# Optimization experiments

Measured on AMD Instinct MI355X. Metric: run time of the kernel, lower is better.

Reference implementation:

```python
import jax, jax.numpy as jnp
import numpy as np

D = 512      # d_model
H = 8        # heads
DK = D // H  # 64
DFF = 2048
EPS = 1e-6


def layer_norm(x, gamma, beta):
    # Faithful to the module: std uses Bessel correction (torch default unbiased)
    # and eps is added to std (not variance); gamma/beta are scalars init to 1.
    m = jnp.mean(x, axis=-1, keepdims=True)
    var = jnp.sum((x - m) ** 2, axis=-1, keepdims=True) / (x.shape[-1] - 1)
    return gamma * (x - m) / (jnp.sqrt(var) + EPS) + beta


def setup_inputs() -> dict:
    key = jax.random.key(0)
    ks = jax.random.split(key, 12)
    s = 0.02
    inp = {
        "x": jax.random.normal(ks[0], (4, 2048, D), dtype=jnp.float32),
        "src_mask": jnp.ones((4, 1, 1, 2048), dtype=jnp.int32),
        "Wq": jax.random.normal(ks[1], (D, D), jnp.float32) * s,
        "bq": jnp.zeros((D,), jnp.float32),
        "Wk": jax.random.normal(ks[2], (D, D), jnp.float32) * s,
        "bk": jnp.zeros((D,), jnp.float32),
        "Wv": jax.random.normal(ks[3], (D, D), jnp.float32) * s,
        "bv": jnp.zeros((D,), jnp.float32),
        "Wo": jax.random.normal(ks[4], (D, D), jnp.float32) * s,
        "bo": jnp.zeros((D,), jnp.float32),
        "W1": jax.random.normal(ks[5], (D, DFF), jnp.float32) * s,
        "b1": jnp.zeros((DFF,), jnp.float32),
        "W2": jax.random.normal(ks[6], (DFF, D), jnp.float32) * s,
        "b2": jnp.zeros((D,), jnp.float32),
        "g1": jnp.ones((), jnp.float32),
        "be1": jnp.ones((), jnp.float32),
        "g2": jnp.ones((), jnp.float32),
        "be2": jnp.ones((), jnp.float32),
    }
    return inp


def reference(x, src_mask, Wq, bq, Wk, bk, Wv, bv, Wo, bo,
              W1, b1, W2, b2, g1, be1, g2, be2):
    B, S, _ = x.shape

    # --- residual 1: pre-LN self-attention ---
    xn = layer_norm(x, g1, be1)                               # [B,S,D]
    q = (xn @ Wq + bq).reshape(B, S, H, DK).transpose(0, 2, 1, 3)  # [B,H,S,DK]
    k = (xn @ Wk + bk).reshape(B, S, H, DK).transpose(0, 2, 1, 3)
    v = (xn @ Wv + bv).reshape(B, S, H, DK).transpose(0, 2, 1, 3)

    scores = jnp.einsum('bhqd,bhkd->bhqk', q, k) / np.float32(np.sqrt(DK))
    scores = jnp.where(src_mask == 0, jnp.float32(-1e9), scores)  # [B,H,S,S]
    attn = jax.nn.softmax(scores, axis=-1)
    o = jnp.einsum('bhqk,bhkd->bhqd', attn, v)                # [B,H,S,DK]
    o = o.transpose(0, 2, 1, 3).reshape(B, S, D)
    x = x + (o @ Wo + bo)

    # --- residual 2: pre-LN feed-forward ---
    xn = layer_norm(x, g2, be2)
    ff = jax.nn.relu(xn @ W1 + b1) @ W2 + b2
    return x + ff
```

## Files before the change

### kernel.cpp

```cpp
#include <hip/hip_runtime.h>
#include <hip/hip_bf16.h>


#define B_   4
#define S_   2048
#define D_   512
#define H_   8
#define DK_  64
#define DFF_ 2048
#define M_   (B_*S_)

typedef __attribute__((ext_vector_type(8))) short short8;
typedef __attribute__((ext_vector_type(4))) float f32x4;
typedef __attribute__((ext_vector_type(16))) float f32x16;

#define QSCALE 0.18033688011f

#if __has_builtin(__builtin_amdgcn_exp2f)
#define EXP2(x) __builtin_amdgcn_exp2f(x)
#else
#define EXP2(x) exp2f(x)
#endif

#define GLOAD_LDS(gp, lp) __builtin_amdgcn_global_load_lds( \
    (const __attribute__((address_space(1))) void*)(gp),    \
    (__attribute__((address_space(3))) void*)(lp), 16, 0, 0)

#define WAITV(N) asm volatile("s_waitcnt vmcnt(" #N ")" ::: "memory")
#define BARRIER() __builtin_amdgcn_s_barrier()

__device__ inline unsigned short f2bf(float f) {
    union { float f; unsigned u; } v; v.f = f;
    unsigned r = v.u + 0x7fffu + ((v.u >> 16) & 1u);
    return (unsigned short)(r >> 16);
}

__device__ inline unsigned cvtpk_bf16(float a, float b) {
    unsigned r;
    asm("v_cvt_pk_bf16_f32 %0, %1, %2" : "=v"(r) : "v"(a), "v"(b));
    return r;
}

__device__ inline void permswap32(unsigned &x, unsigned &y) {
    asm volatile("v_permlane32_swap_b32 %0, %1" : "+v"(x), "+v"(y));
}

__global__ __launch_bounds__(256) void transT_kernel(
    const float* __restrict__ Wq, const float* __restrict__ Wk,
    const float* __restrict__ Wv, const float* __restrict__ Wo,
    const float* __restrict__ W1, const float* __restrict__ W2,
    const float* __restrict__ bq, const float* __restrict__ bk,
    const float* __restrict__ bv, const int* __restrict__ mask,
    float* __restrict__ qkvb, unsigned* __restrict__ mbits,
    short* __restrict__ dst,
    const float* __restrict__ x, const float* __restrict__ g1,
    const float* __restrict__ be1, short* __restrict__ xn) {
    const int id = blockIdx.x, t = threadIdx.x;
    if (id >= 769) {
        int w = t >> 6, l = t & 63;
        int row = (id - 769) * 4 + w;
        const float4* xr = (const float4*)(x + (size_t)row * D_);
        float4 a = xr[l * 2], b = xr[l * 2 + 1];
        float s = a.x + a.y + a.z + a.w + b.x + b.y + b.z + b.w;
        for (int off = 32; off > 0; off >>= 1) s += __shfl_xor(s, off);
        float mean = s * (1.f / 512.f);
        float e[8] = {a.x - mean, a.y - mean, a.z - mean, a.w - mean,
                      b.x - mean, b.y - mean, b.z - mean, b.w - mean};
        float vs = 0.f;
        #pragma unroll
        for (int i = 0; i < 8; i++) vs += e[i] * e[i];
        for (int off = 32; off > 0; off >>= 1) vs += __shfl_xor(vs, off);
        float scale = g1[0] / (sqrtf(vs * (1.f / 511.f)) + 1e-6f);
        float b0 = be1[0];
        union { short8 v; short s[8]; } o;
        #pragma unroll
        for (int i = 0; i < 8; i++) o.s[i] = (short)f2bf(e[i] * scale + b0);
        *(short8*)(xn + (size_t)row * D_ + l * 8) = o.v;
        return;
    }
    if (id == 768) {
        for (int i = t; i < 1536; i += 256)
            qkvb[i] = (i < 512) ? bq[i] * QSCALE : (i < 1024) ? bk[i - 512] : bv[i - 1024];
        if (t < 128) {
            int b = t >> 5, tile = t & 31;
            const int* mr = mask + b * S_ + tile * 64;
            bool all1 = true;
            for (int u = 0; u < 64; u++) all1 &= (mr[u] != 0);
            unsigned long long bal = __ballot(all1);
            if ((t & 63) == 0) {
                mbits[(t >> 6) * 2]     = (unsigned)bal;
                mbits[(t >> 6) * 2 + 1] = (unsigned)(bal >> 32);
            }
        }
        return;
    }
    __shared__ float T[64][65];
    const float* src; short* d; int K, N, tk, tn;
    if (id < 256) {
        int m = id >> 6;
        src = (m == 0) ? Wq : (m == 1) ? Wk : (m == 2) ? Wv : Wo;
        d = dst + (size_t)m * 512 * 512; K = 512; N = 512;
        int j = id & 63; tk = j >> 3; tn = j & 7;
    } else if (id < 512) {
        src = W1; d = dst + (size_t)4 * 512 * 512; K = 512; N = 2048;
        int j = id - 256; tk = j >> 5; tn = j & 31;
    } else {
        src = W2; d = dst + (size_t)4 * 512 * 512 + 2048 * 512; K = 2048; N = 512;
        int j = id - 512; tk = j >> 3; tn = j & 7;
    }
    const int k0 = tk * 64, n0 = tn * 64;
    #pragma unroll
    for (int i = 0; i < 4; i++) {
        int r = i * 16 + (t >> 4), c4 = (t & 15) * 4;
        float4 v = *(const float4*)(src + (size_t)(k0 + r) * N + n0 + c4);
        T[r][c4] = v.x; T[r][c4 + 1] = v.y; T[r][c4 + 2] = v.z; T[r][c4 + 3] = v.w;
    }
    __syncthreads();
    #pragma unroll
    for (int p = 0; p < 2; p++) {
        int j = p * 256 + t, n = j >> 3, kc = (j & 7) * 8;
        union { short8 v; short s[8]; } o;
        #pragma unroll
        for (int u = 0; u < 8; u++) o.s[u] = (short)f2bf(T[kc + u][n]);
        *(short8*)(d + (size_t)(n0 + n) * K + k0 + kc) = o.v;
    }
}

__global__ __launch_bounds__(256) void ln_kernel(const float* __restrict__ x,
                                                 const float* __restrict__ g,
                                                 const float* __restrict__ be,
                                                 short* __restrict__ out) {
    int w = threadIdx.x >> 6, l = threadIdx.x & 63;
    int row = blockIdx.x * 4 + w;
    const float4* xr = (const float4*)(x + (size_t)row * D_);
    float4 a = xr[l * 2], b = xr[l * 2 + 1];
    float s = a.x + a.y + a.z + a.w + b.x + b.y + b.z + b.w;
    for (int off = 32; off > 0; off >>= 1) s += __shfl_xor(s, off);
    float mean = s * (1.f / 512.f);
    float e[8] = {a.x - mean, a.y - mean, a.z - mean, a.w - mean,
                  b.x - mean, b.y - mean, b.z - mean, b.w - mean};
    float vs = 0.f;
    #pragma unroll
    for (int i = 0; i < 8; i++) vs += e[i] * e[i];
    for (int off = 32; off > 0; off >>= 1) vs += __shfl_xor(vs, off);
    float scale = g[0] / (sqrtf(vs * (1.f / 511.f)) + 1e-6f);
    float b0 = be[0];
    union { short8 v; short s[8]; } o;
    #pragma unroll
    for (int i = 0; i < 8; i++) o.s[i] = (short)f2bf(e[i] * scale + b0);
    *(short8*)(out + (size_t)row * D_ + l * 8) = o.v;
}

template <int BN, int MODE>
__global__ __launch_bounds__(256, 2) void gemm_kernel(
    const short* __restrict__ A, const short* __restrict__ Bt,
    const float* __restrict__ bias, const float* __restrict__ resid,
    void* __restrict__ out, int M, int N, int K) {
    constexpr int NF = BN / 32;
    __shared__ __align__(16) short smem[2 * 128 * 64 + 2 * BN * 64];
    auto As = [&](int b) -> short* { return smem + b * 8192; };
    auto Bs = [&](int b) -> short* { return smem + 16384 + b * BN * 64; };
    const int t = threadIdx.x;
    const int w = t >> 6, l = t & 63;
    const int wm = w >> 1, wn = w & 1;
    const int lr = l & 15, lk = l >> 4;
    const int m0 = blockIdx.x * 128, n0 = blockIdx.y * BN;
    f32x4 acc[4][NF] = {};

    auto stage = [&](int buf, int k0) {
        #pragma unroll
        for (int p = 0; p < 4; p++) {
            int id = p * 256 + t;
            int r = id >> 3, c = id & 7, cs = c ^ (r & 7);
            GLOAD_LDS(A + (size_t)(m0 + r) * K + k0 + cs * 8, As(buf) + (p * 256 + w * 64) * 8);
        }
        #pragma unroll
        for (int p = 0; p < BN / 32; p++) {
            int id = p * 256 + t;
            int r = id >> 3, c = id & 7, cs = c ^ (r & 7);
            GLOAD_LDS(Bt + (size_t)(n0 + r) * K + k0 + cs * 8, Bs(buf) + (p * 256 + w * 64) * 8);
        }
    };

    const int nk = K >> 6;
    stage(0, 0);

    for (int tk = 0; tk < nk; ++tk) {
        const int cur = tk & 1;
        if (tk + 1 < nk) {
            stage(cur ^ 1, (tk + 1) * 64);
            if constexpr (BN == 128) WAITV(8); else WAITV(6);
        } else WAITV(0);
        BARRIER();
        short8 af[4][2], bf[NF][2];
        #pragma unroll
        for (int f = 0; f < 4; f++) {
            int ra = wm * 64 + f * 16 + lr;
            #pragma unroll
            for (int kk = 0; kk < 2; kk++)
                af[f][kk] = *(const short8*)&As(cur)[ra * 64 + (((kk * 4 + lk) ^ (ra & 7)) << 3)];
        }
        #pragma unroll
        for (int f = 0; f < NF; f++) {
            int rb = wn * (BN / 2) + f * 16 + lr;
            #pragma unroll
            for (int kk = 0; kk < 2; kk++)
                bf[f][kk] = *(const short8*)&Bs(cur)[rb * 64 + (((kk * 4 + lk) ^ (rb & 7)) << 3)];
        }
        __builtin_amdgcn_s_setprio(1);
        #pragma unroll
        for (int kk = 0; kk < 2; kk++)
            #pragma unroll
            for (int mf = 0; mf < 4; mf++)
                #pragma unroll
                for (int nf = 0; nf < NF; nf++)
                    acc[mf][nf] = __builtin_amdgcn_mfma_f32_16x16x32_bf16(
                        af[mf][kk], bf[nf][kk], acc[mf][nf], 0, 0, 0);
        __builtin_amdgcn_s_setprio(0);
        BARRIER();
    }

    if constexpr (MODE == 0) {
        const int seg = n0 >> 9;
        #pragma unroll
        for (int mf = 0; mf < 4; mf++) {
            #pragma unroll
            for (int nf = 0; nf < NF; nf++) {
                int mb = m0 + wm * 64 + mf * 16 + lk * 4;
                int n  = n0 + wn * (BN / 2) + nf * 16 + lr;
                float bv = bias[n];
                int bb = mb >> 11, sl = mb & 2047, nl = n & 511;
                unsigned short* ob = (unsigned short*)out + (size_t)seg * M_ * D_;
                float v[4];
                #pragma unroll
                for (int i = 0; i < 4; i++) {
                    float val = acc[mf][nf][i];
                    if (seg == 0) val *= QSCALE;
                    v[i] = val + bv;
                }
                if (seg < 2) {
                    #pragma unroll
                    for (int i = 0; i < 4; i++)
                        ob[(((size_t)(bb * 8 + (nl >> 6)) * 2048 + sl + i) << 6) + (nl & 63)] = f2bf(v[i]);
                } else {
                    uint2 pk;
                    pk.x = cvtpk_bf16(v[0], v[1]);
                    pk.y = cvtpk_bf16(v[2], v[3]);
                    *(uint2*)&ob[(((size_t)(bb * 8 + (nl >> 6)) * 64 + (nl & 63)) << 11) + sl] = pk;
                }
            }
        }
    } else if constexpr (MODE == 1) {
        float* E = (float*)smem;
        #pragma unroll
        for (int mf = 0; mf < 4; mf++)
            #pragma unroll
            for (int nf = 0; nf < NF; nf++) {
                int n_loc = wn * (BN / 2) + nf * 16 + lr;
                float bv = bias[n0 + n_loc];
                int c = n_loc >> 4;
                #pragma unroll
                for (int i = 0; i < 4; i++) {
                    int m_loc = wm * 64 + mf * 16 + lk * 4 + i;
                    E[m_loc * 64 + ((c ^ (m_loc & 3)) << 4) + (n_loc & 15)] =
                        acc[mf][nf][i] + bv;
                }
            }
        BARRIER();
        #pragma unroll
        for (int pass = 0; pass < 8; pass++) {
            int fid = pass * 256 + t;
            int row = fid >> 4, c4 = fid & 15;
            int lc = c4 >> 2, j = c4 & 3;
            f32x4 v = *(f32x4*)&E[row * 64 + (((lc ^ (row & 3))) << 4) + j * 4];
            int m = m0 + row, n = n0 + lc * 16 + j * 4;
            f32x4 rv = *(const f32x4*)&resid[(size_t)m * N + n];
            *(f32x4*)&((float*)out)[(size_t)m * N + n] = v + rv;
        }
    } else {
        unsigned short* E16 = (unsigned short*)smem;
        #pragma unroll
        for (int mf = 0; mf < 4; mf++)
            #pragma unroll
            for (int nf = 0; nf < NF; nf++) {
                int n_loc = wn * (BN / 2) + nf * 16 + lr;
                float bv = bias[n0 + n_loc];
                int c = n_loc >> 3;
                #pragma unroll
                for (int i = 0; i < 4; i++) {
                    int m_loc = wm * 64 + mf * 16 + lk * 4 + i;
                    E16[m_loc * 128 + ((c ^ (m_loc & 7)) << 3) + (n_loc & 7)] =
                        f2bf(fmaxf(acc[mf][nf][i] + bv, 0.f));
                }
            }
        BARRIER();
        #pragma unroll
        for (int pass = 0; pass < 8; pass++) {
            int fid = pass * 256 + t;
            int row = fid >> 4, c = fid & 15;
            short8 v = *(short8*)&E16[row * 128 + ((c ^ (row & 7)) << 3)];
            *(short8*)&((unsigned short*)out)[(size_t)(m0 + row) * N + n0 + c * 8] = v;
        }
    }
}

__global__ __launch_bounds__(512, 4) void attn_kernel(
    const short* __restrict__ Q, const short* __restrict__ Kb,
    const short* __restrict__ Vt, const int* __restrict__ mask,
    const unsigned* __restrict__ mbits, unsigned short* __restrict__ O) {
    __shared__ __align__(16) short sm[24576];
    const int t = threadIdx.x, w = t >> 6, l = t & 63;
    const int ql = l & 31, hi = l >> 5;
    const int wh = w >> 2, wl = w & 3;
    const int bh = blockIdx.x, b = bh >> 3, h = bh & 7;
    const int q = blockIdx.y * 128 + wl * 32 + ql;

    const short* qrow = Q + ((size_t)bh * S_ + q) * DK_;
    short8 qf[4];
    #pragma unroll
    for (int s = 0; s < 4; s++) qf[s] = *(const short8*)(qrow + s * 16 + hi * 8);

    const short* kg = Kb + (size_t)bh * S_ * DK_;
    const short* vg = Vt + (size_t)bh * DK_ * S_;
    const int* mrow = mask + b * S_;
    const unsigned mb = mbits[b];

    short* KH = sm + wh * 12288;

    auto stage = [&](int buf, int kv0) {
        short* Kd = KH + buf * 4096;
        short* Vd = Kd + 2048;
        {
            int r = wl * 8 + (l >> 3), c = l & 7, cs = c ^ (r & 7);
            GLOAD_LDS(kg + (size_t)(kv0 + r) * DK_ + cs * 8, &Kd[wl * 512]);
        }
        {
            int r = wl * 8 + (l >> 3), s = l & 7, c = s ^ (r & 7);
            int dk = r + 32 * (c >> 2), kvo = (c & 3) * 8;
            GLOAD_LDS(vg + (size_t)dk * S_ + kv0 + kvo, &Vd[wl * 512]);
        }
    };

    f32x16 o_acc[2] = {};
    float la0 = 0.f, la1 = 0.f, la2 = 0.f, la3 = 0.f;

    stage(0, wh * 1024);
    stage(1, wh * 1024 + 32);
    WAITV(2);
    BARRIER();

    for (int tt = 0; tt < 32; ++tt) {
        const int cur = tt % 3;
        const int gt = wh * 32 + tt;
        if (tt + 2 < 32) stage((tt + 2) % 3, (gt + 2) * 32);
        const short* Ks = KH + cur * 4096;
        const short* Vs = Ks + 2048;

        f32x16 s_acc = {};
        __builtin_amdgcn_s_setprio(1);
        #pragma unroll
        for (int s = 0; s < 4; s++) {
            short8 kf = *(const short8*)&Ks[ql * 64 + (((s * 2 + hi) ^ (ql & 7)) << 3)];
            s_acc = __builtin_amdgcn_mfma_f32_32x32x16_bf16(kf, qf[s], s_acc, 0, 0, 0);
        }
        __builtin_amdgcn_s_setprio(0);

        if (!((mb >> (gt >> 1)) & 1)) {
            #pragma unroll
            for (int r = 0; r < 16; r++) {
                int k = gt * 32 + (r & 3) + 8 * (r >> 2) + 4 * hi;
                if (mrow[k] == 0) s_acc[r] = -1.4426950e9f;
            }
        }

        float p[16];
        #pragma unroll
        for (int r = 0; r < 16; r++) p[r] = EXP2(s_acc[r]);
        #pragma unroll
        for (int r = 0; r < 16; r += 4) {
            la0 += p[r]; la1 += p[r + 1]; la2 += p[r + 2]; la3 += p[r + 3];
        }
        unsigned Dp[8];
        #pragma unroll
        for (int j = 0; j < 8; j++) Dp[j] = cvtpk_bf16(p[2 * j], p[2 * j + 1]);

        #pragma unroll
        for (int s16 = 0; s16 < 2; s16++) {
            unsigned f0 = Dp[s16 * 4 + 0], f1 = Dp[s16 * 4 + 1];
            unsigned f2 = Dp[s16 * 4 + 2], f3 = Dp[s16 * 4 + 3];
            permswap32(f0, f2);
            permswap32(f1, f3);
            union { unsigned u[4]; short8 v; } pu;
            pu.u[0] = f0; pu.u[1] = f1; pu.u[2] = f2; pu.u[3] = f3;
            __builtin_amdgcn_s_setprio(1);
            #pragma unroll
            for (int dt = 0; dt < 2; dt++) {
                short8 vf = *(const short8*)&Vs[ql * 64 + (((dt * 4 + s16 * 2 + hi) ^ (ql & 7)) << 3)];
                o_acc[dt] = __builtin_amdgcn_mfma_f32_32x32x16_bf16(vf, pu.v, o_acc[dt], 0, 0, 0);
            }
            __builtin_amdgcn_s_setprio(0);
        }

        if (tt < 30) WAITV(2); else WAITV(0);
        BARRIER();
    }

    float l_part = (la0 + la1) + (la2 + la3);
    float* C = (float*)sm;
    f32x4* Cv = (f32x4*)sm;
    if (wh == 1) {
        #pragma unroll
        for (int j = 0; j < 8; j++) {
            f32x4 v;
            #pragma unroll
            for (int e = 0; e < 4; e++) v[e] = o_acc[j >> 2][(j & 3) * 4 + e];
            Cv[wl * 512 + j * 64 + l] = v;
        }
        C[8192 + wl * 64 + l] = l_part;
    }
    __syncthreads();
    if (wh == 0) {
        #pragma unroll
        for (int j = 0; j < 8; j++) {
            f32x4 v = Cv[wl * 512 + j * 64 + l];
            #pragma unroll
            for (int e = 0; e < 4; e++) o_acc[j >> 2][(j & 3) * 4 + e] += v[e];
        }
        l_part += C[8192 + wl * 64 + l];
        float linv = 1.f / (l_part + __shfl_xor(l_part, 32));
        unsigned short* orow = O + ((size_t)b * S_ + q) * D_ + h * 64;
        #pragma unroll
        for (int dt = 0; dt < 2; dt++)
            #pragma unroll
            for (int g = 0; g < 4; g++) {
                unsigned u0 = cvtpk_bf16(o_acc[dt][g * 4 + 0] * linv, o_acc[dt][g * 4 + 1] * linv);
                unsigned u1 = cvtpk_bf16(o_acc[dt][g * 4 + 2] * linv, o_acc[dt][g * 4 + 3] * linv);
                uint2 pk; pk.x = u0; pk.y = u1;
                *(uint2*)(orow + dt * 32 + 8 * g + 4 * hi) = pk;
            }
    }
}

extern "C" void kernel_launch(void* const* d_in, const int* in_sizes, int n_in,
                              void* d_out, int out_size, void* d_ws, size_t ws_size,
                              hipStream_t stream) {
    const float* x    = (const float*)d_in[0];
    const int*   mask = (const int*)d_in[1];
    const float* Wq = (const float*)d_in[2];  const float* bq  = (const float*)d_in[3];
    const float* Wk = (const float*)d_in[4];  const float* bk  = (const float*)d_in[5];
    const float* Wv = (const float*)d_in[6];  const float* bv  = (const float*)d_in[7];
    const float* Wo = (const float*)d_in[8];  const float* bo  = (const float*)d_in[9];
    const float* W1 = (const float*)d_in[10]; const float* b1  = (const float*)d_in[11];
    const float* W2 = (const float*)d_in[12]; const float* b2  = (const float*)d_in[13];
    const float* g1 = (const float*)d_in[14]; const float* be1 = (const float*)d_in[15];
    const float* g2 = (const float*)d_in[16]; const float* be2 = (const float*)d_in[17];

    short* WqT = (short*)d_ws;
    short* W1T = WqT + 4 * 512 * 512;
    short* W2T = W1T + 2048 * 512;
    short* xn  = W2T + 512 * 2048;
    short* Qb  = xn  + (size_t)M_ * D_;
    short* Kbf = Qb  + (size_t)M_ * D_;
    short* Vtb = Kbf + (size_t)M_ * D_;
    short* Ob  = Vtb + (size_t)M_ * D_;
    float* x2  = (float*)(Ob + (size_t)M_ * D_);
    float* qkvb = x2;
    unsigned* mbits = (unsigned*)(qkvb + 1536);
    short* WoT = WqT + 3 * 512 * 512;
    short* Hb  = Qb;

    transT_kernel<<<769 + M_ / 4, 256, 0, stream>>>(Wq, Wk, Wv, Wo, W1, W2,
                                                    bq, bk, bv, mask, qkvb, mbits, WqT,
                                                    x, g1, be1, xn);

    gemm_kernel<128, 0><<<dim3(64, 12), 256, 0, stream>>>(xn, WqT, qkvb, nullptr,
                                                          Qb, M_, 1536, 512);

    attn_kernel<<<dim3(B_ * H_, S_ / 128), 512, 0, stream>>>(Qb, Kbf, Vtb, mask, mbits,
                                                             (unsigned short*)Ob);

    gemm_kernel<64, 1><<<dim3(64, 8), 256, 0, stream>>>(Ob, WoT, bo, x, x2, M_, 512, 512);

    ln_kernel<<<M_ / 4, 256, 0, stream>>>(x2, g2, be2, xn);

    gemm_kernel<128, 2><<<dim3(64, 16), 256, 0, stream>>>(xn, W1T, b1, nullptr, Hb, M_, 2048, 512);
    gemm_kernel<64, 1><<<dim3(64, 8), 256, 0, stream>>>(Hb, W2T, b2, x2, (float*)d_out, M_, 512, 2048);
}
```

Measured before the change: 136.6 us.

## Triple-buffer GEMM K loop and stage QKV epilogue through LDS for vector stores

For non-128 BN GEMMs, the K loop now uses three LDS buffers and prefetches two tiles ahead, so global loads have more time to overlap with MFMA work. The QKV projection epilogue for Q and K now writes bf16 results into a swizzled LDS tile first, then each thread stores 16-byte vectors into the head-major layout instead of scattered 2-byte stores. The V path keeps its transposed packed stores. The cost is more LDS per block, which may reduce occupancy, plus an extra barrier in the epilogue.

Result: no change. 137.2 us (+0.5%).

```diff
diff --git a/kernel.cpp b/kernel.cpp
--- a/kernel.cpp
+++ b/kernel.cpp
@@ -157,9 +157,10 @@
     const float* __restrict__ bias, const float* __restrict__ resid,
     void* __restrict__ out, int M, int N, int K) {
     constexpr int NF = BN / 32;
-    __shared__ __align__(16) short smem[2 * 128 * 64 + 2 * BN * 64];
+    constexpr int NBUF = (BN == 128) ? 2 : 3;
+    __shared__ __align__(16) short smem[NBUF * 128 * 64 + NBUF * BN * 64];
     auto As = [&](int b) -> short* { return smem + b * 8192; };
-    auto Bs = [&](int b) -> short* { return smem + 16384 + b * BN * 64; };
+    auto Bs = [&](int b) -> short* { return smem + NBUF * 8192 + b * BN * 64; };
     const int t = threadIdx.x;
     const int w = t >> 6, l = t & 63;
     const int wm = w >> 1, wn = w & 1;
@@ -184,13 +185,20 @@
 
     const int nk = K >> 6;
     stage(0, 0);
+    if constexpr (NBUF == 3) stage(1, 64);
 
     for (int tk = 0; tk < nk; ++tk) {
-        const int cur = tk & 1;
-        if (tk + 1 < nk) {
-            stage(cur ^ 1, (tk + 1) * 64);
-            if constexpr (BN == 128) WAITV(8); else WAITV(6);
-        } else WAITV(0);
+        int cur;
+        if constexpr (NBUF == 2) {
+            cur = tk & 1;
+            if (tk + 1 < nk) { stage(cur ^ 1, (tk + 1) * 64); WAITV(8); }
+            else WAITV(0);
+        } else {
+            cur = tk % 3;
+            if (tk + 2 < nk) { stage((tk + 2) % 3, (tk + 2) * 64); WAITV(12); }
+            else if (tk + 1 < nk) WAITV(6);
+            else WAITV(0);
+        }
         BARRIER();
         short8 af[4][2], bf[NF][2];
         #pragma unroll
@@ -222,30 +230,49 @@
 
     if constexpr (MODE == 0) {
         const int seg = n0 >> 9;
-        #pragma unroll
-        for (int mf = 0; mf < 4; mf++) {
-            #pragma unroll
-            for (int nf = 0; nf < NF; nf++) {
-                int mb = m0 + wm * 64 + mf * 16 + lk * 4;
-                int n  = n0 + wn * (BN / 2) + nf * 16 + lr;
-                float bv = bias[n];
-                int bb = mb >> 11, sl = mb & 2047, nl = n & 511;
-                unsigned short* ob = (unsigned short*)out + (size_t)seg * M_ * D_;
-                float v[4];
+        if (seg < 2) {
+            unsigned short* E16 = (unsigned short*)smem;
+            #pragma unroll
+            for (int mf = 0; mf < 4; mf++)
                 #pragma unroll
-                for (int i = 0; i < 4; i++) {
-                    float val = acc[mf][nf][i];
-                    if (seg == 0) val *= QSCALE;
-                    v[i] = val + bv;
+                for (int nf = 0; nf < NF; nf++) {
+                    int n_loc = wn * (BN / 2) + nf * 16 + lr;
+                    float bv = bias[n0 + n_loc];
+                    int c = n_loc >> 3;
+                    #pragma unroll
+                    for (int i = 0; i < 4; i++) {
+                        int m_loc = wm * 64 + mf * 16 + lk * 4 + i;
+                        float val = acc[mf][nf][i];
+                        if (seg == 0) val *= QSCALE;
+                        E16[m_loc * 128 + ((c ^ (m_loc & 7)) << 3) + (n_loc & 7)] =
+                            f2bf(val + bv);
+                    }
                 }
-                if (seg < 2) {
-                    #pragma unroll
-                    for (int i = 0; i < 4; i++)
-                        ob[(((size_t)(bb * 8 + (nl >> 6)) * 2048 + sl + i) << 6) + (nl & 63)] = f2bf(v[i]);
-                } else {
+            BARRIER();
+            unsigned short* ob = (unsigned short*)out + (size_t)seg * M_ * D_;
+            #pragma unroll
+            for (int pass = 0; pass < 8; pass++) {
+                int fid = pass * 256 + t;
+                int row = fid >> 4, c = fid & 15;
+                short8 v = *(short8*)&E16[row * 128 + ((c ^ (row & 7)) << 3)];
+                int m = m0 + row, n = n0 + c * 8;
+                int bb = m >> 11, sl = m & 2047, nl = n & 511;
+                int h2 = nl >> 6, dk = nl & 63;
+                *(short8*)&ob[(((size_t)(bb * 8 + h2) * 2048 + sl) << 6) + dk] = v;
+            }
+        } else {
+            #pragma unroll
+            for (int mf = 0; mf < 4; mf++) {
+                #pragma unroll
+                for (int nf = 0; nf < NF; nf++) {
+                    int mb = m0 + wm * 64 + mf * 16 + lk * 4;
+                    int n  = n0 + wn * (BN / 2) + nf * 16 + lr;
+                    float bv = bias[n];
+                    int bb = mb >> 11, sl = mb & 2047, nl = n & 511;
+                    unsigned short* ob = (unsigned short*)out + (size_t)2 * M_ * D_;
                     uint2 pk;
-                    pk.x = cvtpk_bf16(v[0], v[1]);
-                    pk.y = cvtpk_bf16(v[2], v[3]);
+                    pk.x = cvtpk_bf16(acc[mf][nf][0] + bv, acc[mf][nf][1] + bv);
+                    pk.y = cvtpk_bf16(acc[mf][nf][2] + bv, acc[mf][nf][3] + bv);
                     *(uint2*)&ob[(((size_t)(bb * 8 + (nl >> 6)) * 64 + (nl & 63)) << 11) + sl] = pk;
                 }
             }
```

## Software-pipeline QK^T one tile ahead with a four-buffer K/V ring

Applied to the files above, without the earlier changes.

The attention loop now computes the QK^T MFMAs for the next KV tile before running masking, exp2 and PV on the current tile, so matrix work can overlap the softmax VALU work. To make room, the K/V staging ring grows from three to four buffers, prefetch runs three tiles ahead, and the wait counts are adjusted to match. In exchange, LDS per block rises from 48KB to 64KB, which may lower the number of resident blocks per CU, and holding an extra 16-float score accumulator adds register pressure.

Result: no change. 136.2 us, median of 2 (-0.3%).

```diff
diff --git a/kernel.cpp b/kernel.cpp
--- a/kernel.cpp
+++ b/kernel.cpp
@@ -308,7 +308,7 @@
     const short* __restrict__ Q, const short* __restrict__ Kb,
     const short* __restrict__ Vt, const int* __restrict__ mask,
     const unsigned* __restrict__ mbits, unsigned short* __restrict__ O) {
-    __shared__ __align__(16) short sm[24576];
+    __shared__ __align__(16) short sm[32768];
     const int t = threadIdx.x, w = t >> 6, l = t & 63;
     const int ql = l & 31, hi = l >> 5;
     const int wh = w >> 2, wl = w & 3;
@@ -325,7 +325,7 @@
     const int* mrow = mask + b * S_;
     const unsigned mb = mbits[b];
 
-    short* KH = sm + wh * 12288;
+    short* KH = sm + wh * 16384;
 
     auto stage = [&](int buf, int kv0) {
         short* Kd = KH + buf * 4096;
@@ -341,41 +341,48 @@
         }
     };
 
+    const f32x16 z16 = {};
+    auto qk = [&](const short* Ks) {
+        short8 kf0 = *(const short8*)&Ks[ql * 64 + ((hi ^ (ql & 7)) << 3)];
+        f32x16 s = __builtin_amdgcn_mfma_f32_32x32x16_bf16(kf0, qf[0], z16, 0, 0, 0);
+        #pragma unroll
+        for (int ss = 1; ss < 4; ss++) {
+            short8 kf = *(const short8*)&Ks[ql * 64 + (((ss * 2 + hi) ^ (ql & 7)) << 3)];
+            s = __builtin_amdgcn_mfma_f32_32x32x16_bf16(kf, qf[ss], s, 0, 0, 0);
+        }
+        return s;
+    };
+
     f32x16 o_acc[2] = {};
     float la0 = 0.f, la1 = 0.f, la2 = 0.f, la3 = 0.f;
 
     stage(0, wh * 1024);
     stage(1, wh * 1024 + 32);
+    stage(2, wh * 1024 + 64);
     WAITV(2);
     BARRIER();
 
+    f32x16 s_cur = qk(KH);
+
     for (int tt = 0; tt < 32; ++tt) {
-        const int cur = tt % 3;
+        const int cur = tt & 3;
         const int gt = wh * 32 + tt;
-        if (tt + 2 < 32) stage((tt + 2) % 3, (gt + 2) * 32);
-        const short* Ks = KH + cur * 4096;
-        const short* Vs = Ks + 2048;
-
-        f32x16 s_acc = {};
-        __builtin_amdgcn_s_setprio(1);
-        #pragma unroll
-        for (int s = 0; s < 4; s++) {
-            short8 kf = *(const short8*)&Ks[ql * 64 + (((s * 2 + hi) ^ (ql & 7)) << 3)];
-            s_acc = __builtin_amdgcn_mfma_f32_32x32x16_bf16(kf, qf[s], s_acc, 0, 0, 0);
-        }
-        __builtin_amdgcn_s_setprio(0);
+        if (tt + 3 < 32) stage((tt + 3) & 3, (gt + 3) * 32);
+
+        f32x16 s_next;
+        if (tt + 1 < 32) s_next = qk(KH + ((tt + 1) & 3) * 4096);
 
         if (!((mb >> (gt >> 1)) & 1)) {
             #pragma unroll
             for (int r = 0; r < 16; r++) {
                 int k = gt * 32 + (r & 3) + 8 * (r >> 2) + 4 * hi;
-                if (mrow[k] == 0) s_acc[r] = -1.4426950e9f;
+                if (mrow[k] == 0) s_cur[r] = -1.4426950e9f;
             }
         }
 
         float p[16];
         #pragma unroll
-        for (int r = 0; r < 16; r++) p[r] = EXP2(s_acc[r]);
+        for (int r = 0; r < 16; r++) p[r] = EXP2(s_cur[r]);
         #pragma unroll
         for (int r = 0; r < 16; r += 4) {
             la0 += p[r]; la1 += p[r + 1]; la2 += p[r + 2]; la3 += p[r + 3];
@@ -384,6 +391,7 @@
         #pragma unroll
         for (int j = 0; j < 8; j++) Dp[j] = cvtpk_bf16(p[2 * j], p[2 * j + 1]);
 
+        const short* Vs = KH + cur * 4096 + 2048;
         #pragma unroll
         for (int s16 = 0; s16 < 2; s16++) {
             unsigned f0 = Dp[s16 * 4 + 0], f1 = Dp[s16 * 4 + 1];
@@ -401,7 +409,8 @@
             __builtin_amdgcn_s_setprio(0);
         }
 
-        if (tt < 30) WAITV(2); else WAITV(0);
+        s_cur = s_next;
+        if (tt < 29) WAITV(2); else WAITV(0);
         BARRIER();
     }
 
```
